# Performance work log

Measured on AMD Instinct MI355X. Metric: run time of the kernel, lower is better.

The kernel has to match this reference:

```python
import jax, jax.numpy as jnp
import numpy as np

NUM_PREFIXES = 64  # == head_dim in this config


def setup_inputs() -> dict:
    key = jax.random.key(0)
    ks = jax.random.split(key, 12)
    B, S, H = 2, 2048, 1024
    hd = NUM_PREFIXES
    nh = H // hd              # 16 heads
    din = dout = 128
    kg = H // dout            # key conv groups = 8
    P = S + hd                # position_dim = 2112
    f = jnp.float32
    sc = 0.02
    hidden = jax.random.normal(ks[0], (B, S, H), f)
    # one-hot positions: prefix tokens (first hd) use slots [S, S+hd), rest use their index
    idx = jnp.where(jnp.arange(S) < hd, S + jnp.arange(S), jnp.arange(S))
    pos = jnp.broadcast_to(jax.nn.one_hot(idx, P, dtype=f)[None], (B, S, P))
    mask = jnp.ones((B, 1, S, S), f)  # peak_into_future=True -> full visibility
    return {
        "hidden_states": hidden,
        "position_embeddings": pos,
        "attention_mask": mask,
        "Wq_head": sc * jax.random.normal(ks[1], (hd, nh, nh), f),
        "Wk_group": sc * jax.random.normal(ks[2], (kg, din, din), f),
        "Wk_head": sc * jax.random.normal(ks[3], (dout, kg, kg), f),
        "Wv_head": sc * jax.random.normal(ks[4], (hd, nh, nh), f),
        "p_attn": sc * jax.random.normal(ks[5], (3 * hd, P), f),
        "p_expand": sc * jax.random.normal(ks[6], (3, 1, nh), f),
        "Wc": sc * jax.random.normal(ks[7], (hd, nh, nh), f),
        "Wg": sc * jax.random.normal(ks[8], (2, H), f),
        "Ug": sc * jax.random.normal(ks[9], (2, H), f),
        "Vg": sc * jax.random.normal(ks[10], (2, P), f),
        "bg": jnp.zeros((2,), f),
    }


def reference(hidden_states, position_embeddings, attention_mask,
              Wq_head, Wk_group, Wk_head, Wv_head,
              p_attn, p_expand, Wc, Wg, Ug, Vg, bg):
    B, S, H = hidden_states.shape
    hd, nh, _ = Wq_head.shape
    kg, din, _ = Wk_group.shape
    npf = NUM_PREFIXES
    # LinearDescent.forward: zero out prefix-prefix attention block
    mask = attention_mask.at[:, :, :npf, :npf].set(0.0)
    # --- Attention: conv2d/per-dim head-mixing projections (proj_conv2d, proj_transpose) ---
    xh = hidden_states.reshape(B, S, nh, hd)
    q = jnp.einsum('bshd,dhg->bsgd', xh, Wq_head)      # per-dim mixing across heads
    v = jnp.einsum('bshd,dhg->bsgd', xh, Wv_head)
    # key path: per-group linear (kg groups of din), then per-dim mixing across groups
    xg = hidden_states.reshape(B, S, kg, din)
    k1 = jnp.einsum('bsgd,gde->bsge', xg, Wk_group)
    k2 = jnp.einsum('bsgd,dgh->bshd', k1, Wk_head)     # (B,S,kg,dout)
    k = k2.reshape(B, S, nh, hd)
    # positional q/k/v via p_attn (3*hd x P) + per-head expansion via p_expand (3,1,nh)
    pqkv = jnp.einsum('bsp,cp->bsc', position_embeddings, p_attn).reshape(B, S, 3, hd)
    q = q + p_expand[0, 0][None, None, :, None] * pqkv[:, :, 0][:, :, None, :]
    k = k + p_expand[1, 0][None, None, :, None] * pqkv[:, :, 1][:, :, None, :]
    v = v + p_expand[2, 0][None, None, :, None] * pqkv[:, :, 2][:, :, None, :]
    # linear (non-softmax) attention with multiplicative mask, no causal mask
    scores = jnp.einsum('bqhd,bkhd->bhqk', q, k) * mask
    ctx = jnp.einsum('bhqk,bkhd->bqhd', scores, v)
    out = jnp.einsum('bqhd,dhg->bqgd', ctx, Wc).reshape(B, S, H)
    # --- Gates: two sigmoid gates from hidden, attention output, and positions ---
    g = jax.nn.sigmoid(hidden_states @ Wg.T + out @ Ug.T + position_embeddings @ Vg.T + bg)
    return g[..., 0:1] * out + g[..., 1:2] * hidden_states
```

## Files before the change

kernel.cpp:

```cpp
#include <hip/hip_runtime.h>
#include <math.h>

#define SS   2048
#define PP   2112
#define C3   192
#define NZCAP 8

__device__ __forceinline__ void fma4s(float4& a, float s, const float4& b) {
    a.x += s*b.x; a.y += s*b.y; a.z += s*b.z; a.w += s*b.w;
}
__device__ __forceinline__ void fme4(float4& a, const float4& x, const float4& w) {
    a.x += x.x*w.x; a.y += x.y*w.y; a.z += x.z*w.z; a.w += x.w*w.w;
}
__device__ __forceinline__ float comp(const float4& v, int j) {
    return j==0 ? v.x : j==1 ? v.y : j==2 ? v.z : v.w;
}
__device__ __forceinline__ float dot4(const float4& a, const float4& b) {
    return a.x*b.x + a.y*b.y + a.z*b.z + a.w*b.w;
}

__global__ __launch_bounds__(256) void k0_prep(
    const float* __restrict__ Wq, const float* __restrict__ Wv,
    const float* __restrict__ Wc, const float* __restrict__ Wkh,
    const float* __restrict__ Wkg, const float* __restrict__ p_attn,
    float* __restrict__ WqT, float* __restrict__ WvT, float* __restrict__ WcT,
    float* __restrict__ WkhT, float* __restrict__ WkgT, float* __restrict__ pT)
{
    const int t = threadIdx.x, blk = blockIdx.x;
    if (blk < 48) {
        const float* src = (blk < 16) ? Wq : (blk < 32) ? Wv : Wc;
        float* dst = (blk < 16) ? WqT : (blk < 32) ? WvT : WcT;
        int base = (blk & 15) * 1024;
        #pragma unroll
        for (int i = 0; i < 4; ++i) {
            int didx = base + i*256 + t;
            int d = didx & 63, g = (didx>>6)&15, h = didx>>10;
            dst[didx] = src[(d<<8)+(h<<4)+g];
        }
    } else if (blk < 56) {
        int base = (blk-48)*1024;
        #pragma unroll
        for (int i = 0; i < 4; ++i) {
            int didx = base + i*256 + t;
            int dk = didx&127, hk = (didx>>7)&7, g = didx>>10;
            WkhT[didx] = Wkh[dk*64 + g*8 + hk];
        }
    } else if (blk < 184) {
        int base = (blk-56)*1024;
        #pragma unroll
        for (int i = 0; i < 4; ++i) {
            int didx = base + i*256 + t;
            int e = didx&127, g = (didx>>7)&7, d = didx>>10;
            WkgT[didx] = Wkg[(g*128+d)*128 + e];
        }
    } else {
        int base = (blk-184)*1024;
        #pragma unroll
        for (int i = 0; i < 4; ++i) {
            int sidx = base + i*256 + t;
            int c = sidx / PP, p = sidx - c*PP;
            pT[p*C3 + c] = p_attn[sidx];
        }
    }
}

__global__ __launch_bounds__(256, 4) void ka_proj(
    const float* __restrict__ hidden, const float* __restrict__ pos,
    const float* __restrict__ WkgT, const float* __restrict__ WkhT,
    const float* __restrict__ WvT,  const float* __restrict__ pT,
    const float* __restrict__ p_exp, const float* __restrict__ Vg,
    float* __restrict__ ko, float* __restrict__ vo,
    float* __restrict__ pq0, float* __restrict__ posg)
{
    __shared__ __align__(16) float xs[8][1024];
    __shared__ __align__(16) float pq[8][C3+4];
    __shared__ int   cnt[8];
    __shared__ int   plist[8][NZCAP];
    __shared__ float vlist[8][NZCAP];

    const int t = threadIdx.x;
    const int row0 = blockIdx.x * 8;

    #pragma unroll
    for (int i = 0; i < 8; ++i)
        ((float4*)xs)[i*256+t] = ((const float4*)hidden)[(size_t)row0*256 + i*256 + t];
    for (int i = t; i < 8*(C3+4); i += 256) ((float*)pq)[i] = 0.f;
    if (t < 8) cnt[t] = 0;
    __syncthreads();

    #pragma unroll
    for (int r = 0; r < 8; ++r) {
        const float4* prow4 = (const float4*)(pos + (size_t)(row0+r)*PP);
        #pragma unroll
        for (int c = 0; c < 3; ++c) {
            int fi = c*256 + t;
            if (fi < PP/4) {
                float4 v4 = prow4[fi];
                float vals[4] = {v4.x, v4.y, v4.z, v4.w};
                #pragma unroll
                for (int u = 0; u < 4; ++u) if (vals[u] != 0.f) {
                    int idx = atomicAdd(&cnt[r], 1);
                    if (idx < NZCAP) { plist[r][idx] = fi*4+u; vlist[r][idx] = vals[u]; }
                    else {
                        int p = fi*4+u; float val = vals[u];
                        for (int cc = 0; cc < C3; ++cc)
                            atomicAdd(&pq[r][cc], val * pT[p*C3+cc]);
                        atomicAdd(&pq[r][C3],   val * Vg[p]);
                        atomicAdd(&pq[r][C3+1], val * Vg[PP+p]);
                    }
                }
            }
        }
    }
    __syncthreads();

    #pragma unroll
    for (int r = 0; r < 8; ++r) {
        int n = min(cnt[r], NZCAP);
        for (int i = 0; i < n; ++i) {
            int p = plist[r][i]; float val = vlist[r][i];
            if (t < C3)           pq[r][t]    += val * pT[p*C3 + t];
            else if (t == C3)     pq[r][C3]   += val * Vg[p];
            else if (t == C3+1)   pq[r][C3+1] += val * Vg[PP+p];
        }
    }
    __syncthreads();

    {
        const int g = t>>4, dq = t&15;
        const float4* WvT4 = (const float4*)WvT;
        const float pev = p_exp[32+g];
        float4 av[8];
        #pragma unroll
        for (int r = 0; r < 8; ++r) {
            av[r] = make_float4(0.f, 0.f, 0.f, 0.f);
            fma4s(av[r], pev, ((const float4*)&pq[r][128])[dq]);
        }
        #pragma unroll 4
        for (int h = 0; h < 16; ++h) {
            float4 w = WvT4[(h*16+g)*16+dq];
            #pragma unroll
            for (int r = 0; r < 8; ++r)
                fme4(av[r], ((const float4*)xs[r])[h*16+dq], w);
        }
        #pragma unroll
        for (int r = 0; r < 8; ++r)
            ((float4*)vo)[(size_t)(row0+r)*256 + g*16 + dq] = av[r];
    }

    float4 a1[8] = {};
    {
        const int g8 = t>>5, eq = t&31;
        const float4* WkgT4 = (const float4*)WkgT;
        for (int dq = 0; dq < 32; ++dq) {
            float4 xq[8];
            #pragma unroll
            for (int r = 0; r < 8; ++r) xq[r] = ((const float4*)xs[r])[g8*32 + dq];
            #pragma unroll
            for (int j = 0; j < 4; ++j) {
                int d = dq*4 + j;
                float4 w = WkgT4[(d*8+g8)*32 + eq];
                #pragma unroll
                for (int r = 0; r < 8; ++r) fma4s(a1[r], comp(xq[r], j), w);
            }
        }
    }
    __syncthreads();
    {
        const int g8 = t>>5, eq = t&31;
        #pragma unroll
        for (int r = 0; r < 8; ++r)
            ((float4*)xs[r])[g8*32 + eq] = a1[r];
    }
    __syncthreads();

    {
        const int hk = t>>5, dkq = t&31;
        const int hh = hk*2 + (dkq>>4);
        const float pe = p_exp[16 + hh];
        const float4* WkhT4 = (const float4*)WkhT;
        float4 acc[8] = {};
        #pragma unroll
        for (int g = 0; g < 8; ++g) {
            float4 w = WkhT4[(g*8+hk)*32 + dkq];
            #pragma unroll
            for (int r = 0; r < 8; ++r)
                fme4(acc[r], ((const float4*)xs[r])[g*32 + dkq], w);
        }
        #pragma unroll
        for (int r = 0; r < 8; ++r) {
            fma4s(acc[r], pe, ((const float4*)&pq[r][64])[dkq&15]);
            ((float4*)ko)[(size_t)(row0+r)*256 + hk*32 + dkq] = acc[r];
        }
    }

    #pragma unroll
    for (int i = 0; i < 2; ++i) {
        int idx = i*256 + t;
        pq0[(size_t)(row0 + (idx>>6))*64 + (idx&63)] = pq[idx>>6][idx&63];
    }
    if (t < 16) posg[(size_t)(row0 + (t>>1))*2 + (t&1)] = pq[t>>1][C3 + (t&1)];
}

__global__ __launch_bounds__(256) void km_kv(
    const float* __restrict__ k, const float* __restrict__ v,
    float* __restrict__ Mpart)
{
    __shared__ __align__(16) float kt[2048];
    __shared__ __align__(16) float vt[2048];
    const int t  = threadIdx.x;
    const int c  = blockIdx.x >> 5;
    const int bh = blockIdx.x & 31;
    const int b  = bh >> 4, h = bh & 15;
    const int et = t>>4, dt = t&15;
    float acc[4][4] = {};

    #pragma unroll
    for (int tile = 0; tile < 2; ++tile) {
        const int r0 = c*64 + tile*32;
        #pragma unroll
        for (int i = 0; i < 2; ++i) {
            int fi = t + 256*i;
            int r = fi>>4, q4 = fi&15;
            size_t ga = (size_t)(b*SS + r0 + r)*256 + h*16 + q4;
            ((float4*)kt)[fi] = ((const float4*)k)[ga];
            ((float4*)vt)[fi] = ((const float4*)v)[ga];
        }
        __syncthreads();
        #pragma unroll 4
        for (int r = 0; r < 32; ++r) {
            float4 kk = ((const float4*)kt)[r*16+et];
            float4 vv = ((const float4*)vt)[r*16+dt];
            float ka[4]={kk.x,kk.y,kk.z,kk.w}, va[4]={vv.x,vv.y,vv.z,vv.w};
            #pragma unroll
            for (int i2=0;i2<4;++i2)
                #pragma unroll
                for (int j=0;j<4;++j) acc[i2][j] += ka[i2]*va[j];
        }
        __syncthreads();
    }
    float4* Mc = (float4*)(Mpart + ((size_t)c*32 + bh)*4096);
    #pragma unroll
    for (int i2=0;i2<4;++i2) {
        float4 o = {acc[i2][0],acc[i2][1],acc[i2][2],acc[i2][3]};
        Mc[(et*4+i2)*16 + dt] = o;
    }
}

__global__ __launch_bounds__(256) void kr_red(
    const float* __restrict__ Mpart,
    float* __restrict__ Mfull, float* __restrict__ Mdiff)
{
    int qid = blockIdx.x*256 + threadIdx.x;
    int bh = qid >> 10, inner = qid & 1023;
    float4 s = {0,0,0,0};
    #pragma unroll
    for (int c = 1; c < 32; ++c) {
        float4 m = ((const float4*)Mpart)[(((size_t)c*32 + bh)<<10) + inner];
        s.x+=m.x; s.y+=m.y; s.z+=m.z; s.w+=m.w;
    }
    ((float4*)Mdiff)[qid] = s;
    float4 m0 = ((const float4*)Mpart)[((size_t)bh<<10) + inner];
    s.x+=m0.x; s.y+=m0.y; s.z+=m0.z; s.w+=m0.w;
    ((float4*)Mfull)[qid] = s;
}

__global__ __launch_bounds__(256, 4) void kb_out(
    const float* __restrict__ hidden, const float* __restrict__ pq0,
    const float* __restrict__ posg,   const float* __restrict__ Mfull,
    const float* __restrict__ Mdiff,  const float* __restrict__ WqT,
    const float* __restrict__ p_exp,  const float* __restrict__ WcT,
    const float* __restrict__ Wg,     const float* __restrict__ Ug,
    const float* __restrict__ bg,     float* __restrict__ yo)
{
    __shared__ __align__(16) float xs[4][1024];
    __shared__ __align__(16) float qs[4][1024];
    __shared__ __align__(16) float pq0s[4][64];
    __shared__ float gs[16];
    const int t  = threadIdx.x;
    const int b  = blockIdx.x >> 9;
    const int s0 = (blockIdx.x & 511) * 4;
    const size_t rqbase = ((size_t)b*SS + s0) * 256;

    float4 xv[4];
    #pragma unroll
    for (int r = 0; r < 4; ++r) {
        xv[r] = ((const float4*)hidden)[rqbase + r*256 + t];
        ((float4*)xs[r])[t] = xv[r];
    }
    if (t < 64) ((float4*)pq0s)[t] = ((const float4*)pq0)[((size_t)b*SS + s0)*16 + t];
    if (t < 16) gs[t] = 0.f;
    __syncthreads();

    const int g = t>>4, dq = t&15;

    float pW0[4], pW1[4];
    {
        float4 w0 = ((const float4*)Wg)[t], w1 = ((const float4*)Wg)[256+t];
        #pragma unroll
        for (int r = 0; r < 4; ++r) {
            pW0[r] = dot4(xv[r], w0);
            pW1[r] = dot4(xv[r], w1);
        }
    }

    {
        const float4* WqT4 = (const float4*)WqT;
        const float peq = p_exp[g];
        float4 aq[4];
        #pragma unroll
        for (int r = 0; r < 4; ++r) {
            aq[r] = make_float4(0.f, 0.f, 0.f, 0.f);
            fma4s(aq[r], peq, ((const float4*)pq0s[r])[dq]);
        }
        #pragma unroll 4
        for (int h = 0; h < 16; ++h) {
            float4 w = WqT4[(h*16+g)*16+dq];
            #pragma unroll
            for (int r = 0; r < 4; ++r)
                fme4(aq[r], ((const float4*)xs[r])[h*16+dq], w);
        }
        #pragma unroll
        for (int r = 0; r < 4; ++r) ((float4*)qs[r])[t] = aq[r];
    }
    __syncthreads();

    {
        const float* Msel = (s0 < 64) ? Mdiff : Mfull;
        const float4* Mb = (const float4*)Msel + ((size_t)b*16 + g)*1024;
        float4 acc[4] = {};
        #pragma unroll 2
        for (int eq = 0; eq < 16; ++eq) {
            float4 qq[4];
            #pragma unroll
            for (int r = 0; r < 4; ++r)
                qq[r] = ((const float4*)qs[r])[g*16 + eq];
            #pragma unroll
            for (int j = 0; j < 4; ++j) {
                float4 m = Mb[(eq*4+j)*16 + dq];
                #pragma unroll
                for (int r = 0; r < 4; ++r) fma4s(acc[r], comp(qq[r],j), m);
            }
        }
        #pragma unroll
        for (int r = 0; r < 4; ++r) ((float4*)xs[r])[t] = acc[r];
    }
    __syncthreads();

    float4 oo[4] = {};
    float pU0[4], pU1[4];
    {
        const float4* WcT4 = (const float4*)WcT;
        #pragma unroll 4
        for (int h = 0; h < 16; ++h) {
            float4 w = WcT4[(h*16+g)*16+dq];
            #pragma unroll
            for (int r = 0; r < 4; ++r)
                fme4(oo[r], ((const float4*)xs[r])[h*16+dq], w);
        }
        float4 u0 = ((const float4*)Ug)[t], u1 = ((const float4*)Ug)[256+t];
        #pragma unroll
        for (int r = 0; r < 4; ++r) {
            pU0[r] = dot4(oo[r], u0);
            pU1[r] = dot4(oo[r], u1);
        }
    }

    #pragma unroll
    for (int r = 0; r < 4; ++r) {
        float v0 = pW0[r], v1 = pW1[r], v2 = pU0[r], v3 = pU1[r];
        #pragma unroll
        for (int off = 32; off > 0; off >>= 1) {
            v0 += __shfl_down(v0, off);
            v1 += __shfl_down(v1, off);
            v2 += __shfl_down(v2, off);
            v3 += __shfl_down(v3, off);
        }
        if ((t & 63) == 0) {
            atomicAdd(&gs[r*4+0], v0);
            atomicAdd(&gs[r*4+1], v1);
            atomicAdd(&gs[r*4+2], v2);
            atomicAdd(&gs[r*4+3], v3);
        }
    }
    __syncthreads();

    #pragma unroll
    for (int r = 0; r < 4; ++r) {
        size_t grow = (size_t)b*SS + s0 + r;
        float z0 = gs[r*4+0] + gs[r*4+2] + posg[grow*2+0] + bg[0];
        float z1 = gs[r*4+1] + gs[r*4+3] + posg[grow*2+1] + bg[1];
        float G0 = 1.f/(1.f+expf(-z0));
        float G1 = 1.f/(1.f+expf(-z1));
        float4 y;
        y.x = G0*oo[r].x + G1*xv[r].x;
        y.y = G0*oo[r].y + G1*xv[r].y;
        y.z = G0*oo[r].z + G1*xv[r].z;
        y.w = G0*oo[r].w + G1*xv[r].w;
        ((float4*)yo)[rqbase + r*256 + t] = y;
    }
}

extern "C" void kernel_launch(void* const* d_in, const int* in_sizes, int n_in,
                              void* d_out, int out_size, void* d_ws, size_t ws_size,
                              hipStream_t stream)
{
    const float* hidden = (const float*)d_in[0];
    const float* pos    = (const float*)d_in[1];
    const float* Wq     = (const float*)d_in[3];
    const float* Wkg    = (const float*)d_in[4];
    const float* Wkh    = (const float*)d_in[5];
    const float* Wv     = (const float*)d_in[6];
    const float* p_attn = (const float*)d_in[7];
    const float* p_exp  = (const float*)d_in[8];
    const float* Wc     = (const float*)d_in[9];
    const float* Wg     = (const float*)d_in[10];
    const float* Ug     = (const float*)d_in[11];
    const float* Vg     = (const float*)d_in[12];
    const float* bg     = (const float*)d_in[13];

    float* ws    = (float*)d_ws;
    float* ko    = ws;
    float* vo    = ws + 4194304;
    float* Mpart = ws + 8388608;
    float* Mfull = ws + 12582912;
    float* Mdiff = ws + 12713984;
    float* pq0   = ws + 12845056;
    float* posg  = ws + 13107200;
    float* WqT   = ws + 13115392;
    float* WvT   = ws + 13131776;
    float* WcT   = ws + 13148160;
    float* WkhT  = ws + 13164544;
    float* WkgT  = ws + 13172736;
    float* pT    = ws + 13303808;

    k0_prep<<<dim3(580), dim3(256), 0, stream>>>(Wq, Wv, Wc, Wkh, Wkg, p_attn,
                                                 WqT, WvT, WcT, WkhT, WkgT, pT);
    ka_proj<<<dim3(512), dim3(256), 0, stream>>>(hidden, pos, WkgT, WkhT, WvT, pT,
                                                 p_exp, Vg, ko, vo, pq0, posg);
    km_kv<<<dim3(1024), dim3(256), 0, stream>>>(ko, vo, Mpart);
    kr_red<<<dim3(128), dim3(256), 0, stream>>>(Mpart, Mfull, Mdiff);
    kb_out<<<dim3(1024), dim3(256), 0, stream>>>(hidden, pq0, posg, Mfull, Mdiff,
                                                 WqT, p_exp, WcT, Wg, Ug, bg, (float*)d_out);
}
```

Measured before the change: 242.2 us.

## Split positional sparse scan into its own kernel and halve projection rows per block

Moves the one-hot position scan and positional q/k/v/gate projection out of ka_proj into a new ks_scan kernel that writes a packed per-row buffer (196 floats) consumed by ka_proj and kb_out. ka_proj now processes 4 rows per block with 1024 blocks instead of 8 rows with 512, aiming for more parallelism and lower register and shared-memory pressure. It adds one extra kernel launch and a global round-trip for the positional results, and it lowers weight reuse per block. The nonzero capacity per row is also raised from 8 to 16.

```diff
diff --git a/kernel.cpp b/kernel.cpp
--- a/kernel.cpp
+++ b/kernel.cpp
@@ -4,7 +4,8 @@
 #define SS   2048
 #define PP   2112
 #define C3   192
-#define NZCAP 8
+#define PQS  196
+#define NZCAP 16
 
 __device__ __forceinline__ void fma4s(float4& a, float s, const float4& b) {
     a.x += s*b.x; a.y += s*b.y; a.z += s*b.z; a.w += s*b.w;
@@ -64,32 +65,23 @@
     }
 }
 
-__global__ __launch_bounds__(256, 4) void ka_proj(
-    const float* __restrict__ hidden, const float* __restrict__ pos,
-    const float* __restrict__ WkgT, const float* __restrict__ WkhT,
-    const float* __restrict__ WvT,  const float* __restrict__ pT,
-    const float* __restrict__ p_exp, const float* __restrict__ Vg,
-    float* __restrict__ ko, float* __restrict__ vo,
-    float* __restrict__ pq0, float* __restrict__ posg)
-{
-    __shared__ __align__(16) float xs[8][1024];
-    __shared__ __align__(16) float pq[8][C3+4];
-    __shared__ int   cnt[8];
-    __shared__ int   plist[8][NZCAP];
-    __shared__ float vlist[8][NZCAP];
-
+__global__ __launch_bounds__(256) void ks_scan(
+    const float* __restrict__ pos, const float* __restrict__ pT,
+    const float* __restrict__ Vg,  float* __restrict__ pqg)
+{
+    __shared__ float pq[4][C3+4];
+    __shared__ int   cnt[4];
+    __shared__ int   plist[4][NZCAP];
+    __shared__ float vlist[4][NZCAP];
     const int t = threadIdx.x;
-    const int row0 = blockIdx.x * 8;
-
-    #pragma unroll
-    for (int i = 0; i < 8; ++i)
-        ((float4*)xs)[i*256+t] = ((const float4*)hidden)[(size_t)row0*256 + i*256 + t];
-    for (int i = t; i < 8*(C3+4); i += 256) ((float*)pq)[i] = 0.f;
-    if (t < 8) cnt[t] = 0;
-    __syncthreads();
-
-    #pragma unroll
-    for (int r = 0; r < 8; ++r) {
+    const int row0 = blockIdx.x * 4;
+
+    for (int i = t; i < 4*(C3+4); i += 256) ((float*)pq)[i] = 0.f;
+    if (t < 4) cnt[t] = 0;
+    __syncthreads();
+
+    #pragma unroll
+    for (int r = 0; r < 4; ++r) {
         const float4* prow4 = (const float4*)(pos + (size_t)(row0+r)*PP);
         #pragma unroll
         for (int c = 0; c < 3; ++c) {
@@ -115,53 +107,70 @@
     __syncthreads();
 
     #pragma unroll
-    for (int r = 0; r < 8; ++r) {
+    for (int r = 0; r < 4; ++r) {
         int n = min(cnt[r], NZCAP);
+        float acc = (t < C3+2) ? pq[r][t] : 0.f;
         for (int i = 0; i < n; ++i) {
             int p = plist[r][i]; float val = vlist[r][i];
-            if (t < C3)           pq[r][t]    += val * pT[p*C3 + t];
-            else if (t == C3)     pq[r][C3]   += val * Vg[p];
-            else if (t == C3+1)   pq[r][C3+1] += val * Vg[PP+p];
-        }
-    }
+            if (t < C3)           acc += val * pT[p*C3 + t];
+            else if (t == C3)     acc += val * Vg[p];
+            else if (t == C3+1)   acc += val * Vg[PP+p];
+        }
+        if (t < C3+2) pqg[(size_t)(row0+r)*PQS + t] = acc;
+    }
+}
+
+__global__ __launch_bounds__(256, 4) void ka_proj(
+    const float* __restrict__ hidden, const float* __restrict__ pqg,
+    const float* __restrict__ WkgT, const float* __restrict__ WkhT,
+    const float* __restrict__ WvT,  const float* __restrict__ p_exp,
+    float* __restrict__ ko, float* __restrict__ vo)
+{
+    __shared__ __align__(16) float xs[4][1024];
+    const int t = threadIdx.x;
+    const int row0 = blockIdx.x * 4;
+
+    #pragma unroll
+    for (int i = 0; i < 4; ++i)
+        ((float4*)xs)[i*256+t] = ((const float4*)hidden)[(size_t)row0*256 + i*256 + t];
     __syncthreads();
 
     {
         const int g = t>>4, dq = t&15;
         const float4* WvT4 = (const float4*)WvT;
         const float pev = p_exp[32+g];
-        float4 av[8];
-        #pragma unroll
-        for (int r = 0; r < 8; ++r) {
-            av[r] = make_float4(0.f, 0.f, 0.f, 0.f);
-            fma4s(av[r], pev, ((const float4*)&pq[r][128])[dq]);
+        float4 av[4];
+        #pragma unroll
+        for (int r = 0; r < 4; ++r) {
+            float4 pv = *(const float4*)(pqg + (size_t)(row0+r)*PQS + 128 + dq*4);
+            av[r] = make_float4(pev*pv.x, pev*pv.y, pev*pv.z, pev*pv.w);
         }
         #pragma unroll 4
         for (int h = 0; h < 16; ++h) {
             float4 w = WvT4[(h*16+g)*16+dq];
             #pragma unroll
-            for (int r = 0; r < 8; ++r)
+            for (int r = 0; r < 4; ++r)
                 fme4(av[r], ((const float4*)xs[r])[h*16+dq], w);
         }
         #pragma unroll
-        for (int r = 0; r < 8; ++r)
+        for (int r = 0; r < 4; ++r)
             ((float4*)vo)[(size_t)(row0+r)*256 + g*16 + dq] = av[r];
     }
 
-    float4 a1[8] = {};
+    float4 a1[4] = {};
     {
         const int g8 = t>>5, eq = t&31;
         const float4* WkgT4 = (const float4*)WkgT;
         for (int dq = 0; dq < 32; ++dq) {
-            float4 xq[8];
-            #pragma unroll
-            for (int r = 0; r < 8; ++r) xq[r] = ((const float4*)xs[r])[g8*32 + dq];
+            float4 xq[4];
+            #pragma unroll
+            for (int r = 0; r < 4; ++r) xq[r] = ((const float4*)xs[r])[g8*32 + dq];
             #pragma unroll
             for (int j = 0; j < 4; ++j) {
                 int d = dq*4 + j;
                 float4 w = WkgT4[(d*8+g8)*32 + eq];
                 #pragma unroll
-                for (int r = 0; r < 8; ++r) fma4s(a1[r], comp(xq[r], j), w);
+                for (int r = 0; r < 4; ++r) fma4s(a1[r], comp(xq[r], j), w);
             }
         }
     }
@@ -169,7 +178,7 @@
     {
         const int g8 = t>>5, eq = t&31;
         #pragma unroll
-        for (int r = 0; r < 8; ++r)
+        for (int r = 0; r < 4; ++r)
             ((float4*)xs[r])[g8*32 + eq] = a1[r];
     }
     __syncthreads();
@@ -179,27 +188,23 @@
         const int hh = hk*2 + (dkq>>4);
         const float pe = p_exp[16 + hh];
         const float4* WkhT4 = (const float4*)WkhT;
-        float4 acc[8] = {};
+        float4 acc[4];
+        #pragma unroll
+        for (int r = 0; r < 4; ++r) {
+            float4 pk = *(const float4*)(pqg + (size_t)(row0+r)*PQS + 64 + (dkq&15)*4);
+            acc[r] = make_float4(pe*pk.x, pe*pk.y, pe*pk.z, pe*pk.w);
+        }
         #pragma unroll
         for (int g = 0; g < 8; ++g) {
             float4 w = WkhT4[(g*8+hk)*32 + dkq];
             #pragma unroll
-            for (int r = 0; r < 8; ++r)
+            for (int r = 0; r < 4; ++r)
                 fme4(acc[r], ((const float4*)xs[r])[g*32 + dkq], w);
         }
         #pragma unroll
-        for (int r = 0; r < 8; ++r) {
-            fma4s(acc[r], pe, ((const float4*)&pq[r][64])[dkq&15]);
+        for (int r = 0; r < 4; ++r)
             ((float4*)ko)[(size_t)(row0+r)*256 + hk*32 + dkq] = acc[r];
-        }
-    }
-
-    #pragma unroll
-    for (int i = 0; i < 2; ++i) {
-        int idx = i*256 + t;
-        pq0[(size_t)(row0 + (idx>>6))*64 + (idx&63)] = pq[idx>>6][idx&63];
-    }
-    if (t < 16) posg[(size_t)(row0 + (t>>1))*2 + (t&1)] = pq[t>>1][C3 + (t&1)];
+    }
 }
 
 __global__ __launch_bounds__(256) void km_kv(
@@ -266,12 +271,12 @@
 }
 
 __global__ __launch_bounds__(256, 4) void kb_out(
-    const float* __restrict__ hidden, const float* __restrict__ pq0,
-    const float* __restrict__ posg,   const float* __restrict__ Mfull,
-    const float* __restrict__ Mdiff,  const float* __restrict__ WqT,
-    const float* __restrict__ p_exp,  const float* __restrict__ WcT,
-    const float* __restrict__ Wg,     const float* __restrict__ Ug,
-    const float* __restrict__ bg,     float* __restrict__ yo)
+    const float* __restrict__ hidden, const float* __restrict__ pqg,
+    const float* __restrict__ Mfull,  const float* __restrict__ Mdiff,
+    const float* __restrict__ WqT,    const float* __restrict__ p_exp,
+    const float* __restrict__ WcT,    const float* __restrict__ Wg,
+    const float* __restrict__ Ug,     const float* __restrict__ bg,
+    float* __restrict__ yo)
 {
     __shared__ __align__(16) float xs[4][1024];
     __shared__ __align__(16) float qs[4][1024];
@@ -288,7 +293,10 @@
         xv[r] = ((const float4*)hidden)[rqbase + r*256 + t];
         ((float4*)xs[r])[t] = xv[r];
     }
-    if (t < 64) ((float4*)pq0s)[t] = ((const float4*)pq0)[((size_t)b*SS + s0)*16 + t];
+    if (t < 64) {
+        int r = t>>4, q = t&15;
+        ((float4*)pq0s[r])[q] = *(const float4*)(pqg + (size_t)(b*SS + s0 + r)*PQS + q*4);
+    }
     if (t < 16) gs[t] = 0.f;
     __syncthreads();
 
@@ -388,8 +396,8 @@
     #pragma unroll
     for (int r = 0; r < 4; ++r) {
         size_t grow = (size_t)b*SS + s0 + r;
-        float z0 = gs[r*4+0] + gs[r*4+2] + posg[grow*2+0] + bg[0];
-        float z1 = gs[r*4+1] + gs[r*4+3] + posg[grow*2+1] + bg[1];
+        float z0 = gs[r*4+0] + gs[r*4+2] + pqg[grow*PQS + 192] + bg[0];
+        float z1 = gs[r*4+1] + gs[r*4+3] + pqg[grow*PQS + 193] + bg[1];
         float G0 = 1.f/(1.f+expf(-z0));
         float G1 = 1.f/(1.f+expf(-z1));
         float4 y;
@@ -425,21 +433,22 @@
     float* Mpart = ws + 8388608;
     float* Mfull = ws + 12582912;
     float* Mdiff = ws + 12713984;
-    float* pq0   = ws + 12845056;
-    float* posg  = ws + 13107200;
-    float* WqT   = ws + 13115392;
-    float* WvT   = ws + 13131776;
-    float* WcT   = ws + 13148160;
-    float* WkhT  = ws + 13164544;
-    float* WkgT  = ws + 13172736;
-    float* pT    = ws + 13303808;
+    float* pqg   = ws + 12845056;
+    float* WqT   = ws + 13647872;
+    float* WvT   = ws + 13664256;
+    float* WcT   = ws + 13680640;
+    float* WkhT  = ws + 13697024;
+    float* WkgT  = ws + 13705216;
+    float* pT    = ws + 13836288;
 
     k0_prep<<<dim3(580), dim3(256), 0, stream>>>(Wq, Wv, Wc, Wkh, Wkg, p_attn,
                                                  WqT, WvT, WcT, WkhT, WkgT, pT);
-    ka_proj<<<dim3(512), dim3(256), 0, stream>>>(hidden, pos, WkgT, WkhT, WvT, pT,
-                                                 p_exp, Vg, ko, vo, pq0, posg);
+    ks_scan<<<dim3(1024), dim3(256), 0, stream>>>(pos, pT, Vg, pqg);
+    ka_proj<<<dim3(1024), dim3(256), 0, stream>>>(hidden, pqg, WkgT, WkhT, WvT,
+                                                  p_exp, ko, vo);
     km_kv<<<dim3(1024), dim3(256), 0, stream>>>(ko, vo, Mpart);
     kr_red<<<dim3(128), dim3(256), 0, stream>>>(Mpart, Mfull, Mdiff);
-    kb_out<<<dim3(1024), dim3(256), 0, stream>>>(hidden, pq0, posg, Mfull, Mdiff,
-                                                 WqT, p_exp, WcT, Wg, Ug, bg, (float*)d_out);
-}
+    kb_out<<<dim3(1024), dim3(256), 0, stream>>>(hidden, pqg, Mfull, Mdiff,
+                                                 WqT, p_exp, WcT, Wg, Ug, bg,
+                                                 (float*)d_out);
+}
```

Result: faster. 222.0 us (-8.3%).
